# Optimization experiments

Hardware: AMD Instinct MI355X
Metric: run time of the kernel (lower is better)

Reference implementation:

```python
import jax, jax.numpy as jnp
import numpy as np

B, N, D_IN, H, L, NH, PE, DEG, OUT = 8, 1024, 128, 256, 4, 8, 8, 16, 1
BN = B * N
E = BN * DEG
DH = H // NH
EPS = 1e-5


def _gelu(x):
    return jax.nn.gelu(x, approximate=False)  # torch nn.GELU default (erf)


def _bn(x, g, b):
    # BatchNorm1d in training mode: batch mean / biased variance over node dim
    m = x.mean(axis=0)
    v = x.var(axis=0)
    return (x - m) * jax.lax.rsqrt(v + EPS) * g + b


def setup_inputs() -> dict:
    key = jax.random.key(0)
    ks = jax.random.split(key, 30)
    s = 0.05
    x = jax.random.normal(ks[0], (BN, D_IN), jnp.float32)
    # block-diagonal COO adjacency: edges stay within each graph's node block
    base = jnp.repeat(jnp.arange(B, dtype=jnp.int32) * N, N * DEG)
    edge_row = base + jax.random.randint(ks[1], (E,), 0, N, jnp.int32)
    edge_col = base + jax.random.randint(ks[2], (E,), 0, N, jnp.int32)
    edge_val = jax.random.uniform(ks[3], (E,), jnp.float32) / DEG
    batch_pe = jax.random.normal(ks[4], (BN, PE), jnp.float32)
    p = {
        'W_in': jax.random.normal(ks[5], (H, D_IN)) * s,
        'b_in': jnp.zeros((H,)),
        'W_pe': jax.random.normal(ks[6], (H, PE)) * s,
        'b_pe': jnp.zeros((H,)),
        'gcn_W': jax.random.normal(ks[7], (L, H, H)) * s,
        'attn_in_W': jax.random.normal(ks[8], (L, 3 * H, H)) * s,
        'attn_in_b': jnp.zeros((L, 3 * H)),
        'attn_out_W': jax.random.normal(ks[9], (L, H, H)) * s,
        'attn_out_b': jnp.zeros((L, H)),
        'bn_g': jnp.ones((L, 3, H)),
        'bn_b': jnp.zeros((L, 3, H)),
        'ffn_W1': jax.random.normal(ks[10], (L, 4 * H, H)) * s,
        'ffn_b1': jnp.zeros((L, 4 * H)),
        'ffn_W2': jax.random.normal(ks[11], (L, H, 4 * H)) * s,
        'ffn_b2': jnp.zeros((L, H)),
        'head_W1': jax.random.normal(ks[12], (H // 2, H)) * s,
        'head_b1': jnp.zeros((H // 2,)),
        'head_W2': jax.random.normal(ks[13], (OUT, H // 2)) * s,
        'head_b2': jnp.zeros((OUT,)),
    }
    p = {k: v.astype(jnp.float32) for k, v in p.items()}
    return dict(x=x, edge_row=edge_row, edge_col=edge_col, edge_val=edge_val,
                batch_pe=batch_pe, **p)


def reference(x, edge_row, edge_col, edge_val, batch_pe,
              W_in, b_in, W_pe, b_pe,
              gcn_W, attn_in_W, attn_in_b, attn_out_W, attn_out_b,
              bn_g, bn_b, ffn_W1, ffn_b1, ffn_W2, ffn_b2,
              head_W1, head_b1, head_W2, head_b2):
    h = x @ W_in.T + b_in + batch_pe @ W_pe.T + b_pe  # (BN, H)
    scale = 1.0 / jnp.sqrt(jnp.asarray(DH, h.dtype))
    for l in range(L):
        # local GCN: linear -> sparse mm (block-diag COO) -> GELU
        msg = edge_val[:, None] * (h @ gcn_W[l].T)[edge_col]  # (E, H)
        h_local = _gelu(jax.ops.segment_sum(msg, edge_row, num_segments=BN))
        h = _bn(h + h_local, bn_g[l, 0], bn_b[l, 0])
        # global self-attention over each graph's N nodes
        hh = h.reshape(B, N, H)
        qkv = hh @ attn_in_W[l].T + attn_in_b[l]  # (B, N, 3H)
        q, k, v = [t.reshape(B, N, NH, DH) for t in jnp.split(qkv, 3, axis=-1)]
        att = jax.nn.softmax(jnp.einsum('bqhd,bkhd->bhqk', q, k) * scale, axis=-1)
        o = jnp.einsum('bhqk,bkhd->bqhd', att, v).reshape(B, N, H)
        o = (o @ attn_out_W[l].T + attn_out_b[l]).reshape(BN, H)
        h = _bn(h + o, bn_g[l, 1], bn_b[l, 1])
        # FFN
        f = _gelu(h @ ffn_W1[l].T + ffn_b1[l]) @ ffn_W2[l].T + ffn_b2[l]
        h = _bn(h + f, bn_g[l, 2], bn_b[l, 2])
    out = jax.nn.sigmoid(_gelu(h @ head_W1.T + head_b1) @ head_W2.T + head_b2)
    return out
```

## Files before the change

kernel.cpp:

```cpp
#include <hip/hip_runtime.h>
#include <hip/hip_bf16.h>
#include <math.h>

#define BB 8
#define NN 1024
#define BN 8192
#define D_IN 128
#define HH 256
#define LL 4
#define NHD 8
#define DH 32
#define EE 131072
#define EPSV 1e-5f

typedef unsigned short u16;
typedef unsigned int u32;
typedef __attribute__((ext_vector_type(8))) short bf16x8;
typedef __attribute__((ext_vector_type(4))) float f32x4;

__device__ __forceinline__ float gelu_erf(float x) {
    return 0.5f * x * (1.0f + erff(x * 0.70710678118654752f));
}

__device__ __forceinline__ u16 f2bf(float v) {
    __hip_bfloat16 b = __float2bfloat16(v);
    return *reinterpret_cast<u16*>(&b);
}

__device__ __forceinline__ float bf2f(u16 u) {
    u32 x = ((u32)u) << 16;
    return __builtin_bit_cast(float, x);
}

__device__ __forceinline__ u32 pack2bf(float lo, float hi) {
    return ((u32)f2bf(hi) << 16) | (u32)f2bf(lo);
}

__global__ __launch_bounds__(256) void cast_all_kernel(
        const float* s0, const float* s1, const float* s2, const float* s3,
        const float* s4, const float* s5, const float* s6, const float* s7,
        u16* d0, u16* d1, u16* d2, u16* d3, u16* d4, u16* d5, u16* d6, u16* d7) {
    int blk = blockIdx.x;
    const float* s; u16* d; int base;
    if      (blk < 1024) { s = s0; d = d0; base = 0; }
    else if (blk < 1056) { s = s1; d = d1; base = 1024; }
    else if (blk < 1312) { s = s2; d = d2; base = 1056; }
    else if (blk < 2080) { s = s3; d = d3; base = 1312; }
    else if (blk < 2336) { s = s4; d = d4; base = 2080; }
    else if (blk < 3360) { s = s5; d = d5; base = 2336; }
    else if (blk < 4384) { s = s6; d = d6; base = 3360; }
    else                 { s = s7; d = d7; base = 4384; }
    int i = (blk - base) * 256 + threadIdx.x;
    float4 v = ((const float4*)s)[i];
    ushort4 o;
    o.x = f2bf(v.x); o.y = f2bf(v.y); o.z = f2bf(v.z); o.w = f2bf(v.w);
    ((ushort4*)d)[i] = o;
}

__global__ __launch_bounds__(256) void hist_kernel(const int* __restrict__ edge_row,
                                                   int* __restrict__ counts) {
    int e = blockIdx.x * 256 + threadIdx.x;
    atomicAdd(&counts[edge_row[e]], 1);
}

__global__ __launch_bounds__(256) void prefix_kernel(const int* __restrict__ counts,
                                                     int* __restrict__ row_start,
                                                     int* __restrict__ cursor) {
    __shared__ int lds[256];
    int t = threadIdx.x;
    int local[32];
    int s = 0;
#pragma unroll
    for (int i = 0; i < 32; ++i) { local[i] = counts[t * 32 + i]; s += local[i]; }
    lds[t] = s;
    __syncthreads();
    for (int off = 1; off < 256; off <<= 1) {
        int v = (t >= off) ? lds[t - off] : 0;
        __syncthreads();
        lds[t] += v;
        __syncthreads();
    }
    int excl = (t == 0) ? 0 : lds[t - 1];
#pragma unroll
    for (int i = 0; i < 32; ++i) {
        int c = local[i];
        row_start[t * 32 + i] = excl;
        cursor[t * 32 + i] = excl;
        excl += c;
    }
    if (t == 255) row_start[8192] = excl;
}

__global__ __launch_bounds__(256) void scatter_kernel(const int* __restrict__ edge_row,
                                                      int* __restrict__ cursor,
                                                      int* __restrict__ csr_e) {
    int e = blockIdx.x * 256 + threadIdx.x;
    int r = edge_row[e];
    int pos = atomicAdd(&cursor[r], 1);
    csr_e[pos] = e;
}

__global__ __launch_bounds__(256) void gcn_gather_kernel(const u16* __restrict__ t1b,
                                                         const int* __restrict__ row_start,
                                                         const int* __restrict__ csr_e,
                                                         const int* __restrict__ edge_col,
                                                         const float* __restrict__ edge_val,
                                                         float* __restrict__ outb) {
    int wave = threadIdx.x >> 6;
    int lane = threadIdx.x & 63;
    int r = blockIdx.x * 4 + wave;
    float a0 = 0.f, a1 = 0.f, a2 = 0.f, a3 = 0.f;
    int p0 = row_start[r], p1 = row_start[r + 1];
    for (int p = p0; p < p1; ++p) {
        int e = csr_e[p];
        int c = edge_col[e];
        float v = edge_val[e];
        ushort4 sv = *(const ushort4*)&t1b[(size_t)c * HH + lane * 4];
        a0 += v * bf2f(sv.x); a1 += v * bf2f(sv.y);
        a2 += v * bf2f(sv.z); a3 += v * bf2f(sv.w);
    }
    float4 g;
    g.x = gelu_erf(a0); g.y = gelu_erf(a1); g.z = gelu_erf(a2); g.w = gelu_erf(a3);
    *(float4*)&outb[(size_t)r * HH + lane * 4] = g;
}

__global__ __launch_bounds__(256) void bn_reduce_atomic_kernel(float* __restrict__ h,
                                                               const float* __restrict__ add,
                                                               float* __restrict__ S,
                                                               float* __restrict__ Q) {
    int c = threadIdx.x;
    int r0 = blockIdx.x * 32;
    float s = 0.f, q = 0.f;
#pragma unroll 4
    for (int i = 0; i < 32; ++i) {
        int idx = (r0 + i) * HH + c;
        float v = h[idx] + add[idx];
        h[idx] = v;
        s += v; q += v * v;
    }
    atomicAdd(&S[c], s);
    atomicAdd(&Q[c], q);
}

__global__ __launch_bounds__(256) void bn_apply_kernel(float* __restrict__ h,
                                                       u16* __restrict__ hb,
                                                       const float* __restrict__ S,
                                                       const float* __restrict__ Q,
                                                       const float* __restrict__ g,
                                                       const float* __restrict__ b,
                                                       float* __restrict__ Zs,
                                                       float* __restrict__ Zq) {
    int i = blockIdx.x * 256 + threadIdx.x;
    float4 v = ((float4*)h)[i];
    int c4 = (i & 63) * 4;
    float o0, o1, o2, o3;
    {
        float mean = S[c4 + 0] * (1.f / 8192.f);
        float var = Q[c4 + 0] * (1.f / 8192.f) - mean * mean;
        float sc = g[c4 + 0] * rsqrtf(var + EPSV);
        o0 = v.x * sc + (b[c4 + 0] - mean * sc);
    }
    {
        float mean = S[c4 + 1] * (1.f / 8192.f);
        float var = Q[c4 + 1] * (1.f / 8192.f) - mean * mean;
        float sc = g[c4 + 1] * rsqrtf(var + EPSV);
        o1 = v.y * sc + (b[c4 + 1] - mean * sc);
    }
    {
        float mean = S[c4 + 2] * (1.f / 8192.f);
        float var = Q[c4 + 2] * (1.f / 8192.f) - mean * mean;
        float sc = g[c4 + 2] * rsqrtf(var + EPSV);
        o2 = v.z * sc + (b[c4 + 2] - mean * sc);
    }
    {
        float mean = S[c4 + 3] * (1.f / 8192.f);
        float var = Q[c4 + 3] * (1.f / 8192.f) - mean * mean;
        float sc = g[c4 + 3] * rsqrtf(var + EPSV);
        o3 = v.w * sc + (b[c4 + 3] - mean * sc);
    }
    float4 ov; ov.x = o0; ov.y = o1; ov.z = o2; ov.w = o3;
    ((float4*)h)[i] = ov;
    ushort4 o;
    o.x = f2bf(o0); o.y = f2bf(o1); o.z = f2bf(o2); o.w = f2bf(o3);
    ((ushort4*)hb)[i] = o;
    if (blockIdx.x == 0) {
        Zs[threadIdx.x] = 0.f;
        Zq[threadIdx.x] = 0.f;
    }
}

#define SWZ(row, c8) ((c8) ^ (((row) & 7) << 3))
template <int EPI, int OUTMODE>
__global__ __launch_bounds__(256) void gemm_mfma(const u16* __restrict__ A,
                                                 const u16* __restrict__ W,
                                                 const float* __restrict__ bias,
                                                 void* __restrict__ Cout,
                                                 int M, int K, int N,
                                                 float* __restrict__ psumF,
                                                 float* __restrict__ psqF) {
    __shared__ u16 As[128][64];
    __shared__ u16 Ws[64][64];
    int t = threadIdx.x;
    int bm = blockIdx.y * 128, bn = blockIdx.x * 64;
    int wid = t >> 6, lane = t & 63;
    int wr = wid >> 1, wc = wid & 1;
    int lr = lane & 15, lg = lane >> 4;

    f32x4 zero = {0.f, 0.f, 0.f, 0.f};
    f32x4 acc[4][2];
#pragma unroll
    for (int mi = 0; mi < 4; ++mi)
#pragma unroll
        for (int ni = 0; ni < 2; ++ni) acc[mi][ni] = zero;

    int sr = t >> 3;
    int c8 = (t & 7) * 8;

    for (int k0 = 0; k0 < K; k0 += 64) {
        __syncthreads();
#pragma unroll
        for (int p = 0; p < 4; ++p) {
            int row = sr + p * 32;
            const u16* src = A + (size_t)(bm + row) * K + k0 + c8;
            *(int4*)&As[row][SWZ(row, c8)] = *(const int4*)src;
        }
#pragma unroll
        for (int p = 0; p < 2; ++p) {
            int row = sr + p * 32;
            const u16* src = W + (size_t)(bn + row) * K + k0 + c8;
            *(int4*)&Ws[row][SWZ(row, c8)] = *(const int4*)src;
        }
        __syncthreads();
#pragma unroll
        for (int kk = 0; kk < 2; ++kk) {
            bf16x8 af[4], bf[2];
#pragma unroll
            for (int mi = 0; mi < 4; ++mi) {
                int row = wr * 64 + mi * 16 + lr;
                af[mi] = *(const bf16x8*)&As[row][SWZ(row, kk * 32 + lg * 8)];
            }
#pragma unroll
            for (int ni = 0; ni < 2; ++ni) {
                int row = wc * 32 + ni * 16 + lr;
                bf[ni] = *(const bf16x8*)&Ws[row][SWZ(row, kk * 32 + lg * 8)];
            }
#pragma unroll
            for (int mi = 0; mi < 4; ++mi)
#pragma unroll
                for (int ni = 0; ni < 2; ++ni)
                    acc[mi][ni] = __builtin_amdgcn_mfma_f32_16x16x32_bf16(af[mi], bf[ni], acc[mi][ni], 0, 0, 0);
        }
    }

    if (OUTMODE == 2) {
#pragma unroll
        for (int ni = 0; ni < 2; ++ni) {
            int col = bn + wc * 32 + ni * 16 + lr;
            float bj = bias[col];
            float s = 0.f, q = 0.f;
#pragma unroll
            for (int mi = 0; mi < 4; ++mi) {
#pragma unroll
                for (int r = 0; r < 4; ++r) {
                    int row = bm + wr * 64 + mi * 16 + lg * 4 + r;
                    float* hp = (float*)Cout + (size_t)row * N + col;
                    float nv = *hp + acc[mi][ni][r] + bj;
                    *hp = nv;
                    s += nv; q += nv * nv;
                }
            }
            s += __shfl_xor(s, 16); s += __shfl_xor(s, 32);
            q += __shfl_xor(q, 16); q += __shfl_xor(q, 32);
            if (lg == 0) {
                atomicAdd(&psumF[col], s);
                atomicAdd(&psqF[col], q);
            }
        }
    } else {
#pragma unroll
        for (int ni = 0; ni < 2; ++ni) {
            int col = bn + wc * 32 + ni * 16 + lr;
            float bj = bias ? bias[col] : 0.f;
#pragma unroll
            for (int mi = 0; mi < 4; ++mi) {
#pragma unroll
                for (int r = 0; r < 4; ++r) {
                    int row = bm + wr * 64 + mi * 16 + lg * 4 + r;
                    float v = acc[mi][ni][r] + bj;
                    if (EPI == 1) v = gelu_erf(v);
                    if (OUTMODE == 1)
                        ((u16*)Cout)[(size_t)row * N + col] = f2bf(v);
                    else
                        ((float*)Cout)[(size_t)row * N + col] = v;
                }
            }
        }
    }
}

template <int EPI, int OUTBF>
__global__ __launch_bounds__(256) void gemm_mfma2(const u16* __restrict__ A,
                                                  const u16* __restrict__ W,
                                                  const float* __restrict__ bias,
                                                  void* __restrict__ Cout,
                                                  int M, int K, int N) {
    __shared__ u16 As[128][64];
    __shared__ u16 Ws[128][64];
    int t = threadIdx.x;
    int bm = blockIdx.y * 128, bn = blockIdx.x * 128;
    int wid = t >> 6, lane = t & 63;
    int wr = wid >> 1, wc = wid & 1;
    int lr = lane & 15, lg = lane >> 4;

    f32x4 zero = {0.f, 0.f, 0.f, 0.f};
    f32x4 acc[4][4];
#pragma unroll
    for (int mi = 0; mi < 4; ++mi)
#pragma unroll
        for (int ni = 0; ni < 4; ++ni) acc[mi][ni] = zero;

    int sr = t >> 3;
    int c8 = (t & 7) * 8;

    for (int k0 = 0; k0 < K; k0 += 64) {
        __syncthreads();
#pragma unroll
        for (int p = 0; p < 4; ++p) {
            int row = sr + p * 32;
            const u16* srcA = A + (size_t)(bm + row) * K + k0 + c8;
            *(int4*)&As[row][SWZ(row, c8)] = *(const int4*)srcA;
            const u16* srcW = W + (size_t)(bn + row) * K + k0 + c8;
            *(int4*)&Ws[row][SWZ(row, c8)] = *(const int4*)srcW;
        }
        __syncthreads();
#pragma unroll
        for (int kk = 0; kk < 2; ++kk) {
            bf16x8 af[4], bf[4];
#pragma unroll
            for (int mi = 0; mi < 4; ++mi) {
                int row = wr * 64 + mi * 16 + lr;
                af[mi] = *(const bf16x8*)&As[row][SWZ(row, kk * 32 + lg * 8)];
            }
#pragma unroll
            for (int ni = 0; ni < 4; ++ni) {
                int row = wc * 64 + ni * 16 + lr;
                bf[ni] = *(const bf16x8*)&Ws[row][SWZ(row, kk * 32 + lg * 8)];
            }
#pragma unroll
            for (int mi = 0; mi < 4; ++mi)
#pragma unroll
                for (int ni = 0; ni < 4; ++ni)
                    acc[mi][ni] = __builtin_amdgcn_mfma_f32_16x16x32_bf16(af[mi], bf[ni], acc[mi][ni], 0, 0, 0);
        }
    }

#pragma unroll
    for (int ni = 0; ni < 4; ++ni) {
        int col = bn + wc * 64 + ni * 16 + lr;
        float bj = bias ? bias[col] : 0.f;
#pragma unroll
        for (int mi = 0; mi < 4; ++mi) {
#pragma unroll
            for (int r = 0; r < 4; ++r) {
                int row = bm + wr * 64 + mi * 16 + lg * 4 + r;
                float v = acc[mi][ni][r] + bj;
                if (EPI == 1) v = gelu_erf(v);
                if (OUTBF)
                    ((u16*)Cout)[(size_t)row * N + col] = f2bf(v);
                else
                    ((float*)Cout)[(size_t)row * N + col] = v;
            }
        }
    }
}

__global__ __launch_bounds__(256) void pe_add_kernel(const float* __restrict__ pe,
                                                     const float* __restrict__ Wpe,
                                                     const float* __restrict__ bpe,
                                                     float* __restrict__ h,
                                                     u16* __restrict__ hb) {
    __shared__ float Ws[8][256];
    int t = threadIdx.x;
    for (int i = t; i < 2048; i += 256) Ws[i & 7][i >> 3] = Wpe[i];
    __syncthreads();
    int w = t >> 6, lane = t & 63;
    int r = blockIdx.x * 4 + w;
    const float* pr = pe + r * 8;
    float p[8];
#pragma unroll
    for (int k = 0; k < 8; ++k) p[k] = pr[k];
    int c0 = lane * 4;
    float4 hv = *(float4*)&h[(size_t)r * HH + c0];
    float o0 = hv.x + bpe[c0 + 0], o1 = hv.y + bpe[c0 + 1];
    float o2 = hv.z + bpe[c0 + 2], o3 = hv.w + bpe[c0 + 3];
#pragma unroll
    for (int k = 0; k < 8; ++k) {
        o0 += p[k] * Ws[k][c0 + 0];
        o1 += p[k] * Ws[k][c0 + 1];
        o2 += p[k] * Ws[k][c0 + 2];
        o3 += p[k] * Ws[k][c0 + 3];
    }
    float4 ov; ov.x = o0; ov.y = o1; ov.z = o2; ov.w = o3;
    *(float4*)&h[(size_t)r * HH + c0] = ov;
    ushort4 ob;
    ob.x = f2bf(o0); ob.y = f2bf(o1); ob.z = f2bf(o2); ob.w = f2bf(o3);
    *(ushort4*)&hb[(size_t)r * HH + c0] = ob;
}

__global__ __launch_bounds__(256) void vtrans_kernel(const u16* __restrict__ qkv,
                                                     u16* __restrict__ vT) {
    __shared__ u16 Ls[64][64];
    int bid = blockIdx.x;
    int kt = bid & 15;
    int head = (bid >> 4) & 7;
    int b = bid >> 7;
    int t = threadIdx.x;
    int key_l = t >> 2, blkS = t & 3;
    const u16* src = qkv + (size_t)(b * NN + kt * 64 + key_l) * 768 + 512 + head * DH + blkS * 8;
    int sb = (blkS ^ (key_l & 7) ^ ((key_l >> 3) & 7)) * 8;
    *(int4*)&Ls[key_l][sb] = *(const int4*)src;
    __syncthreads();
    int d = t >> 3, kc = t & 7;
    union { u16 a[8]; int4 v; } tmp;
#pragma unroll
    for (int j = 0; j < 8; ++j) {
        int col = (((d >> 3) ^ j ^ kc) << 3) | (d & 7);
        tmp.a[j] = Ls[kc * 8 + j][col];
    }
    u16* dst = vT + (size_t)((b * 8 + head) * 32 + d) * NN + kt * 64 + kc * 8;
    *(int4*)dst = tmp.v;
}

__global__ __launch_bounds__(256) void attn_mfma_kernel(const u16* __restrict__ qkv,
                                                        const u16* __restrict__ vT,
                                                        u16* __restrict__ o) {
    __shared__ __align__(16) u16 Ks[64][40];
    __shared__ __align__(16) u16 Vt[32][72];
    __shared__ __align__(16) u16 Ot[64][40];
    int bid = blockIdx.x;
    int qt = bid & 15;
    int head = (bid >> 4) & 7;
    int b = bid >> 7;
    int t = threadIdx.x;
    int w = t >> 6, lane = t & 63;
    int lr = lane & 15, lg = lane >> 4;

    bf16x8 qf;
    {
        const u16* qsrc = qkv + (size_t)(b * NN + qt * 64 + w * 16 + lr) * 768 + head * DH + lg * 8;
        bf16x8 raw = *(const bf16x8*)qsrc;
#pragma unroll
        for (int j = 0; j < 8; ++j) {
            float f = bf2f((u16)raw[j]) * 0.17677669529663689f;
            qf[j] = (short)f2bf(f);
        }
    }

    f32x4 zero = {0.f, 0.f, 0.f, 0.f};
    f32x4 oacc[2] = {zero, zero};
    float m = -1e30f, l = 0.f;

    int srow = t >> 2, sc8 = (t & 3) * 8;
    int vd = t >> 3, vc8 = (t & 7) * 8;
    const u16* kbase = qkv + (size_t)(b * NN) * 768 + 256 + head * DH + sc8;
    const u16* vbase = vT + (size_t)((b * 8 + head) * 32 + vd) * NN + vc8;

    int srcA = ((lg & 1) << 5) + lr;
    int srcB = srcA + 16;
    int hi = lg >> 1;

    for (int k0 = 0; k0 < NN; k0 += 64) {
        __syncthreads();
        *(int4*)&Ks[srow][sc8] = *(const int4*)(kbase + (size_t)(k0 + srow) * 768);
        *(int4*)&Vt[vd][vc8] = *(const int4*)(vbase + k0);
        __syncthreads();

        f32x4 st[4];
#pragma unroll
        for (int kt = 0; kt < 4; ++kt) {
            bf16x8 kf = *(const bf16x8*)&Ks[kt * 16 + lr][lg * 8];
            st[kt] = __builtin_amdgcn_mfma_f32_16x16x32_bf16(kf, qf, zero, 0, 0, 0);
        }

        float tm = -1e30f;
#pragma unroll
        for (int kt = 0; kt < 4; ++kt)
#pragma unroll
            for (int r = 0; r < 4; ++r) tm = fmaxf(tm, st[kt][r]);
        tm = fmaxf(tm, __shfl_xor(tm, 16));
        tm = fmaxf(tm, __shfl_xor(tm, 32));
        float mn = fmaxf(m, tm);
        float corr = __expf(m - mn);
        l *= corr;
#pragma unroll
        for (int dh = 0; dh < 2; ++dh)
#pragma unroll
            for (int r = 0; r < 4; ++r) oacc[dh][r] *= corr;

        float ps = 0.f;
        u32 pw0[4], pw1[4];
#pragma unroll
        for (int kt = 0; kt < 4; ++kt) {
            float p0 = __expf(st[kt][0] - mn);
            float p1 = __expf(st[kt][1] - mn);
            float p2 = __expf(st[kt][2] - mn);
            float p3 = __expf(st[kt][3] - mn);
            ps += (p0 + p1) + (p2 + p3);
            pw0[kt] = pack2bf(p0, p1);
            pw1[kt] = pack2bf(p2, p3);
        }
        ps += __shfl_xor(ps, 16);
        ps += __shfl_xor(ps, 32);
        l += ps;
        m = mn;

#pragma unroll
        for (int c = 0; c < 2; ++c) {
            u32 w0a = (u32)__shfl((int)pw0[c * 2], srcA);
            u32 w0b = (u32)__shfl((int)pw0[c * 2 + 1], srcA);
            u32 w1a = (u32)__shfl((int)pw1[c * 2], srcA);
            u32 w1b = (u32)__shfl((int)pw1[c * 2 + 1], srcA);
            u32 w2a = (u32)__shfl((int)pw0[c * 2], srcB);
            u32 w2b = (u32)__shfl((int)pw0[c * 2 + 1], srcB);
            u32 w3a = (u32)__shfl((int)pw1[c * 2], srcB);
            u32 w3b = (u32)__shfl((int)pw1[c * 2 + 1], srcB);
            union { bf16x8 v; u32 u[4]; } pf;
            pf.u[0] = hi ? w0b : w0a;
            pf.u[1] = hi ? w1b : w1a;
            pf.u[2] = hi ? w2b : w2a;
            pf.u[3] = hi ? w3b : w3a;
#pragma unroll
            for (int dh = 0; dh < 2; ++dh) {
                bf16x8 vf = *(const bf16x8*)&Vt[dh * 16 + lr][c * 32 + lg * 8];
                oacc[dh] = __builtin_amdgcn_mfma_f32_16x16x32_bf16(vf, pf.v, oacc[dh], 0, 0, 0);
            }
        }
    }

    float inv = 1.f / l;
    __syncthreads();
#pragma unroll
    for (int dh = 0; dh < 2; ++dh)
#pragma unroll
        for (int r = 0; r < 4; ++r)
            Ot[w * 16 + lr][dh * 16 + lg * 4 + r] = f2bf(oacc[dh][r] * inv);
    __syncthreads();
    {
        int orow = t >> 2, oc8 = (t & 3) * 8;
        u16* dst = o + (size_t)(b * NN + qt * 64 + orow) * HH + head * DH + oc8;
        *(int4*)dst = *(const int4*)&Ot[orow][oc8];
    }
}

__global__ __launch_bounds__(256) void head2_kernel(const float* __restrict__ g1,
                                                    const float* __restrict__ W2,
                                                    const float* __restrict__ b2,
                                                    float* __restrict__ out) {
    __shared__ float w[128];
    int t = threadIdx.x;
    if (t < 128) w[t] = W2[t];
    __syncthreads();
    int r = blockIdx.x * 256 + t;
    float s = b2[0];
    const float* row = g1 + (size_t)r * 128;
#pragma unroll
    for (int k = 0; k < 128; k += 4) {
        float4 v = *(const float4*)&row[k];
        s += v.x * w[k] + v.y * w[k + 1] + v.z * w[k + 2] + v.w * w[k + 3];
    }
    out[r] = 1.f / (1.f + __expf(-s));
}

extern "C" void kernel_launch(void* const* d_in, const int* in_sizes, int n_in,
                              void* d_out, int out_size, void* d_ws, size_t ws_size,
                              hipStream_t stream) {
    const float* x        = (const float*)d_in[0];
    const int*   edge_row = (const int*)d_in[1];
    const int*   edge_col = (const int*)d_in[2];
    const float* edge_val = (const float*)d_in[3];
    const float* pe       = (const float*)d_in[4];
    const float* W_in     = (const float*)d_in[5];
    const float* b_in     = (const float*)d_in[6];
    const float* W_pe     = (const float*)d_in[7];
    const float* b_pe     = (const float*)d_in[8];
    const float* gcn_W    = (const float*)d_in[9];
    const float* attn_in_W  = (const float*)d_in[10];
    const float* attn_in_b  = (const float*)d_in[11];
    const float* attn_out_W = (const float*)d_in[12];
    const float* attn_out_b = (const float*)d_in[13];
    const float* bn_g     = (const float*)d_in[14];
    const float* bn_b     = (const float*)d_in[15];
    const float* ffn_W1   = (const float*)d_in[16];
    const float* ffn_b1   = (const float*)d_in[17];
    const float* ffn_W2   = (const float*)d_in[18];
    const float* ffn_b2   = (const float*)d_in[19];
    const float* head_W1  = (const float*)d_in[20];
    const float* head_b1  = (const float*)d_in[21];
    const float* head_W2  = (const float*)d_in[22];
    const float* head_b2  = (const float*)d_in[23];
    float* out = (float*)d_out;

    float* w = (float*)d_ws;
    float* h    = w; w += 2097152;
    float* buf1 = w; w += 8388608;
    float* buf2 = w; w += 2097152;
    int* counts    = (int*)w; w += 8192;
    float* bnstats = w; w += 1024;
    int* row_start = (int*)w; w += 8224;
    int* cursor    = (int*)w; w += 8192;
    int* csr_e     = (int*)w; w += 131072;
    u16* hb   = (u16*)w;
    u16* xb   = hb + 2097152;
    u16* aob  = xb + 1048576;
    u16* wbWin = aob + 2097152;
    u16* wbGcn = wbWin + 32768;
    u16* wbAin = wbGcn + 262144;
    u16* wbAout = wbAin + 786432;
    u16* wbF1  = wbAout + 262144;
    u16* wbF2  = wbF1 + 1048576;
    u16* wbH1  = wbF2 + 1048576;
    u16* t1b  = (u16*)buf1;
    u16* qkvb = (u16*)buf1;
    u16* midb = (u16*)buf1;
    u16* vT   = (u16*)buf1 + 12582912;

    auto Sp = [&](int k) { return bnstats + (k & 1) * 512; };
    auto Qp = [&](int k) { return bnstats + (k & 1) * 512 + 256; };

    hipMemsetAsync(counts, 0, (8192 + 1024) * sizeof(int), stream);
    hist_kernel<<<512, 256, 0, stream>>>(edge_row, counts);
    prefix_kernel<<<1, 256, 0, stream>>>(counts, row_start, cursor);
    scatter_kernel<<<512, 256, 0, stream>>>(edge_row, cursor, csr_e);

    cast_all_kernel<<<4416, 256, 0, stream>>>(
        x, W_in, gcn_W, attn_in_W, attn_out_W, ffn_W1, ffn_W2, head_W1,
        xb, wbWin, wbGcn, wbAin, wbAout, wbF1, wbF2, wbH1);

    gemm_mfma<0, 0><<<dim3(4, 64), 256, 0, stream>>>(xb, wbWin, b_in, h, BN, D_IN, HH, bnstats, bnstats);
    pe_add_kernel<<<2048, 256, 0, stream>>>(pe, W_pe, b_pe, h, hb);

    for (int l = 0; l < LL; ++l) {
        int k1 = l * 3, k2 = l * 3 + 1, k3 = l * 3 + 2;

        gemm_mfma<0, 1><<<dim3(4, 64), 256, 0, stream>>>(hb, wbGcn + l * 65536, nullptr, t1b, BN, HH, HH, bnstats, bnstats);
        gcn_gather_kernel<<<2048, 256, 0, stream>>>(t1b, row_start, csr_e, edge_col, edge_val, buf2);
        bn_reduce_atomic_kernel<<<256, 256, 0, stream>>>(h, buf2, Sp(k1), Qp(k1));
        bn_apply_kernel<<<2048, 256, 0, stream>>>(h, hb, Sp(k1), Qp(k1),
            bn_g + (l * 3 + 0) * 256, bn_b + (l * 3 + 0) * 256, Sp(k1 + 1), Qp(k1 + 1));

        gemm_mfma2<0, 1><<<dim3(6, 64), 256, 0, stream>>>(hb, wbAin + l * 196608, attn_in_b + l * 768, qkvb, BN, HH, 768);
        vtrans_kernel<<<1024, 256, 0, stream>>>(qkvb, vT);
        attn_mfma_kernel<<<1024, 256, 0, stream>>>(qkvb, vT, aob);
        gemm_mfma<0, 2><<<dim3(4, 64), 256, 0, stream>>>(aob, wbAout + l * 65536, attn_out_b + l * 256, h, BN, HH, HH, Sp(k2), Qp(k2));
        bn_apply_kernel<<<2048, 256, 0, stream>>>(h, hb, Sp(k2), Qp(k2),
            bn_g + (l * 3 + 1) * 256, bn_b + (l * 3 + 1) * 256, Sp(k2 + 1), Qp(k2 + 1));

        gemm_mfma2<1, 1><<<dim3(8, 64), 256, 0, stream>>>(hb, wbF1 + l * 262144, ffn_b1 + l * 1024, midb, BN, HH, 1024);
        gemm_mfma<0, 2><<<dim3(4, 64), 256, 0, stream>>>(midb, wbF2 + l * 262144, ffn_b2 + l * 256, h, BN, 1024, HH, Sp(k3), Qp(k3));
        bn_apply_kernel<<<2048, 256, 0, stream>>>(h, hb, Sp(k3), Qp(k3),
            bn_g + (l * 3 + 2) * 256, bn_b + (l * 3 + 2) * 256, Sp(k3 + 1), Qp(k3 + 1));
    }

    gemm_mfma<1, 0><<<dim3(2, 64), 256, 0, stream>>>(hb, wbH1, head_b1, buf1, BN, HH, 128, bnstats, bnstats);
    head2_kernel<<<32, 256, 0, stream>>>(buf1, head_W2, head_b2, out);
}
```

Measured before the change: 847.4 us.

## Fuse BatchNorm apply into GEMM prologues/epilogues and GCN gather, lazy softmax rescale

Removes the standalone bn_apply and bn_reduce passes and the bf16 copy of h. Normalization of the previous BN is now done lazily: the GEMM A-tile loads read fp32 h, apply the scale and shift, and convert to bf16. Residual epilogues apply the pending normalization to h before adding, and the GCN gather fuses residual, normalization and stats accumulation. Attention switches to raw v_exp_f32 with log2e folded into the q scale, and only rescales the running max when it grows by more than 8. The cost is reading fp32 A (twice the bytes), recomputing BN coefficients per tile, and a less parallel per-channel gather loop.

```diff
diff --git a/kernel.cpp b/kernel.cpp
--- a/kernel.cpp
+++ b/kernel.cpp
@@ -34,6 +34,12 @@
 
 __device__ __forceinline__ u32 pack2bf(float lo, float hi) {
     return ((u32)f2bf(hi) << 16) | (u32)f2bf(lo);
+}
+
+__device__ __forceinline__ float exp2_fast(float x) {
+    float r;
+    asm("v_exp_f32 %0, %1" : "=v"(r) : "v"(x));
+    return r;
 }
 
 __global__ __launch_bounds__(256) void cast_all_kernel(
@@ -100,107 +106,66 @@
     csr_e[pos] = e;
 }
 
-__global__ __launch_bounds__(256) void gcn_gather_kernel(const u16* __restrict__ t1b,
-                                                         const int* __restrict__ row_start,
-                                                         const int* __restrict__ csr_e,
-                                                         const int* __restrict__ edge_col,
-                                                         const float* __restrict__ edge_val,
-                                                         float* __restrict__ outb) {
-    int wave = threadIdx.x >> 6;
-    int lane = threadIdx.x & 63;
-    int r = blockIdx.x * 4 + wave;
-    float a0 = 0.f, a1 = 0.f, a2 = 0.f, a3 = 0.f;
-    int p0 = row_start[r], p1 = row_start[r + 1];
-    for (int p = p0; p < p1; ++p) {
-        int e = csr_e[p];
-        int c = edge_col[e];
-        float v = edge_val[e];
-        ushort4 sv = *(const ushort4*)&t1b[(size_t)c * HH + lane * 4];
-        a0 += v * bf2f(sv.x); a1 += v * bf2f(sv.y);
-        a2 += v * bf2f(sv.z); a3 += v * bf2f(sv.w);
-    }
-    float4 g;
-    g.x = gelu_erf(a0); g.y = gelu_erf(a1); g.z = gelu_erf(a2); g.w = gelu_erf(a3);
-    *(float4*)&outb[(size_t)r * HH + lane * 4] = g;
-}
-
-__global__ __launch_bounds__(256) void bn_reduce_atomic_kernel(float* __restrict__ h,
-                                                               const float* __restrict__ add,
-                                                               float* __restrict__ S,
-                                                               float* __restrict__ Q) {
+__global__ __launch_bounds__(256) void gather_bn_kernel(const u16* __restrict__ t1b,
+                                                        const int* __restrict__ row_start,
+                                                        const int* __restrict__ csr_e,
+                                                        const int* __restrict__ edge_col,
+                                                        const float* __restrict__ edge_val,
+                                                        float* __restrict__ h,
+                                                        const float* __restrict__ Sa,
+                                                        const float* __restrict__ Qa,
+                                                        const float* __restrict__ ga,
+                                                        const float* __restrict__ ba,
+                                                        float* __restrict__ So,
+                                                        float* __restrict__ Qo) {
     int c = threadIdx.x;
-    int r0 = blockIdx.x * 32;
+    float sc = 1.f, sh = 0.f;
+    if (Sa) {
+        float mean = Sa[c] * (1.f / 8192.f);
+        float var = Qa[c] * (1.f / 8192.f) - mean * mean;
+        float rs = rsqrtf(var + EPSV);
+        sc = ga[c] * rs;
+        sh = ba[c] - mean * sc;
+    }
+    int r0 = blockIdx.x * 8;
     float s = 0.f, q = 0.f;
-#pragma unroll 4
-    for (int i = 0; i < 32; ++i) {
-        int idx = (r0 + i) * HH + c;
-        float v = h[idx] + add[idx];
-        h[idx] = v;
-        s += v; q += v * v;
-    }
-    atomicAdd(&S[c], s);
-    atomicAdd(&Q[c], q);
-}
-
-__global__ __launch_bounds__(256) void bn_apply_kernel(float* __restrict__ h,
-                                                       u16* __restrict__ hb,
-                                                       const float* __restrict__ S,
-                                                       const float* __restrict__ Q,
-                                                       const float* __restrict__ g,
-                                                       const float* __restrict__ b,
-                                                       float* __restrict__ Zs,
-                                                       float* __restrict__ Zq) {
-    int i = blockIdx.x * 256 + threadIdx.x;
-    float4 v = ((float4*)h)[i];
-    int c4 = (i & 63) * 4;
-    float o0, o1, o2, o3;
-    {
-        float mean = S[c4 + 0] * (1.f / 8192.f);
-        float var = Q[c4 + 0] * (1.f / 8192.f) - mean * mean;
-        float sc = g[c4 + 0] * rsqrtf(var + EPSV);
-        o0 = v.x * sc + (b[c4 + 0] - mean * sc);
-    }
-    {
-        float mean = S[c4 + 1] * (1.f / 8192.f);
-        float var = Q[c4 + 1] * (1.f / 8192.f) - mean * mean;
-        float sc = g[c4 + 1] * rsqrtf(var + EPSV);
-        o1 = v.y * sc + (b[c4 + 1] - mean * sc);
-    }
-    {
-        float mean = S[c4 + 2] * (1.f / 8192.f);
-        float var = Q[c4 + 2] * (1.f / 8192.f) - mean * mean;
-        float sc = g[c4 + 2] * rsqrtf(var + EPSV);
-        o2 = v.z * sc + (b[c4 + 2] - mean * sc);
-    }
-    {
-        float mean = S[c4 + 3] * (1.f / 8192.f);
-        float var = Q[c4 + 3] * (1.f / 8192.f) - mean * mean;
-        float sc = g[c4 + 3] * rsqrtf(var + EPSV);
-        o3 = v.w * sc + (b[c4 + 3] - mean * sc);
-    }
-    float4 ov; ov.x = o0; ov.y = o1; ov.z = o2; ov.w = o3;
-    ((float4*)h)[i] = ov;
-    ushort4 o;
-    o.x = f2bf(o0); o.y = f2bf(o1); o.z = f2bf(o2); o.w = f2bf(o3);
-    ((ushort4*)hb)[i] = o;
-    if (blockIdx.x == 0) {
-        Zs[threadIdx.x] = 0.f;
-        Zq[threadIdx.x] = 0.f;
-    }
+#pragma unroll
+    for (int i = 0; i < 8; ++i) {
+        int r = r0 + i;
+        int p0 = row_start[r], p1 = row_start[r + 1];
+        float a = 0.f;
+        for (int p = p0; p < p1; ++p) {
+            int e = csr_e[p];
+            float v = edge_val[e];
+            a += v * bf2f(t1b[(size_t)edge_col[e] * HH + c]);
+        }
+        size_t idx = (size_t)r * HH + c;
+        float nv = h[idx] * sc + sh + gelu_erf(a);
+        h[idx] = nv;
+        s += nv; q += nv * nv;
+    }
+    atomicAdd(&So[c], s);
+    atomicAdd(&Qo[c], q);
 }
 
 #define SWZ(row, c8) ((c8) ^ (((row) & 7) << 3))
-template <int EPI, int OUTMODE>
-__global__ __launch_bounds__(256) void gemm_mfma(const u16* __restrict__ A,
-                                                 const u16* __restrict__ W,
-                                                 const float* __restrict__ bias,
-                                                 void* __restrict__ Cout,
-                                                 int M, int K, int N,
-                                                 float* __restrict__ psumF,
-                                                 float* __restrict__ psqF) {
+template <int EPI, int OUTMODE, int NORMA>
+__global__ __launch_bounds__(256) void gemm_mfma(
+        const void* __restrict__ Ain, const u16* __restrict__ W,
+        const float* __restrict__ bias, void* __restrict__ Cout,
+        int M, int K, int N,
+        const float* __restrict__ Sa, const float* __restrict__ Qa,
+        const float* __restrict__ ga, const float* __restrict__ ba,
+        const float* __restrict__ Sr, const float* __restrict__ Qr,
+        const float* __restrict__ gr, const float* __restrict__ br,
+        float* __restrict__ So, float* __restrict__ Qo,
+        float* __restrict__ Zs, float* __restrict__ Zq) {
     __shared__ u16 As[128][64];
     __shared__ u16 Ws[64][64];
     int t = threadIdx.x;
+    if (Zs != nullptr && blockIdx.x == 0 && blockIdx.y == 0) {
+        Zs[t] = 0.f; Zq[t] = 0.f;
+    }
     int bm = blockIdx.y * 128, bn = blockIdx.x * 64;
     int wid = t >> 6, lane = t & 63;
     int wr = wid >> 1, wc = wid & 1;
@@ -218,11 +183,46 @@
 
     for (int k0 = 0; k0 < K; k0 += 64) {
         __syncthreads();
-#pragma unroll
-        for (int p = 0; p < 4; ++p) {
-            int row = sr + p * 32;
-            const u16* src = A + (size_t)(bm + row) * K + k0 + c8;
-            *(int4*)&As[row][SWZ(row, c8)] = *(const int4*)src;
+        if (NORMA) {
+            float scj[8], shj[8];
+            if (Sa) {
+#pragma unroll
+                for (int j = 0; j < 8; ++j) {
+                    int ch = k0 + c8 + j;
+                    float mean = Sa[ch] * (1.f / 8192.f);
+                    float var = Qa[ch] * (1.f / 8192.f) - mean * mean;
+                    float rs = rsqrtf(var + EPSV);
+                    scj[j] = ga[ch] * rs;
+                    shj[j] = ba[ch] - mean * scj[j];
+                }
+            } else {
+#pragma unroll
+                for (int j = 0; j < 8; ++j) { scj[j] = 1.f; shj[j] = 0.f; }
+            }
+#pragma unroll
+            for (int p = 0; p < 4; ++p) {
+                int row = sr + p * 32;
+                const float* src = (const float*)Ain + (size_t)(bm + row) * K + k0 + c8;
+                float4 a0 = *(const float4*)src;
+                float4 a1 = *(const float4*)(src + 4);
+                union { u16 a[8]; int4 v; } pk;
+                pk.a[0] = f2bf(a0.x * scj[0] + shj[0]);
+                pk.a[1] = f2bf(a0.y * scj[1] + shj[1]);
+                pk.a[2] = f2bf(a0.z * scj[2] + shj[2]);
+                pk.a[3] = f2bf(a0.w * scj[3] + shj[3]);
+                pk.a[4] = f2bf(a1.x * scj[4] + shj[4]);
+                pk.a[5] = f2bf(a1.y * scj[5] + shj[5]);
+                pk.a[6] = f2bf(a1.z * scj[6] + shj[6]);
+                pk.a[7] = f2bf(a1.w * scj[7] + shj[7]);
+                *(int4*)&As[row][SWZ(row, c8)] = pk.v;
+            }
+        } else {
+#pragma unroll
+            for (int p = 0; p < 4; ++p) {
+                int row = sr + p * 32;
+                const u16* src = (const u16*)Ain + (size_t)(bm + row) * K + k0 + c8;
+                *(int4*)&As[row][SWZ(row, c8)] = *(const int4*)src;
+            }
         }
 #pragma unroll
         for (int p = 0; p < 2; ++p) {
@@ -256,7 +256,11 @@
 #pragma unroll
         for (int ni = 0; ni < 2; ++ni) {
             int col = bn + wc * 32 + ni * 16 + lr;
-            float bj = bias[col];
+            float mean = Sr[col] * (1.f / 8192.f);
+            float var = Qr[col] * (1.f / 8192.f) - mean * mean;
+            float rs = rsqrtf(var + EPSV);
+            float scr = gr[col] * rs;
+            float shr = br[col] - mean * scr + bias[col];
             float s = 0.f, q = 0.f;
 #pragma unroll
             for (int mi = 0; mi < 4; ++mi) {
@@ -264,7 +268,7 @@
                 for (int r = 0; r < 4; ++r) {
                     int row = bm + wr * 64 + mi * 16 + lg * 4 + r;
                     float* hp = (float*)Cout + (size_t)row * N + col;
-                    float nv = *hp + acc[mi][ni][r] + bj;
+                    float nv = (*hp) * scr + shr + acc[mi][ni][r];
                     *hp = nv;
                     s += nv; q += nv * nv;
                 }
@@ -272,8 +276,8 @@
             s += __shfl_xor(s, 16); s += __shfl_xor(s, 32);
             q += __shfl_xor(q, 16); q += __shfl_xor(q, 32);
             if (lg == 0) {
-                atomicAdd(&psumF[col], s);
-                atomicAdd(&psqF[col], q);
+                atomicAdd(&So[col], s);
+                atomicAdd(&Qo[col], q);
             }
         }
     } else {
@@ -298,15 +302,20 @@
     }
 }
 
-template <int EPI, int OUTBF>
-__global__ __launch_bounds__(256) void gemm_mfma2(const u16* __restrict__ A,
-                                                  const u16* __restrict__ W,
-                                                  const float* __restrict__ bias,
-                                                  void* __restrict__ Cout,
-                                                  int M, int K, int N) {
+template <int EPI, int OUTBF, int NORMA>
+__global__ __launch_bounds__(256) void gemm_mfma2(
+        const void* __restrict__ Ain, const u16* __restrict__ W,
+        const float* __restrict__ bias, void* __restrict__ Cout,
+        int M, int K, int N,
+        const float* __restrict__ Sa, const float* __restrict__ Qa,
+        const float* __restrict__ ga, const float* __restrict__ ba,
+        float* __restrict__ Zs, float* __restrict__ Zq) {
     __shared__ u16 As[128][64];
     __shared__ u16 Ws[128][64];
     int t = threadIdx.x;
+    if (Zs != nullptr && blockIdx.x == 0 && blockIdx.y == 0) {
+        Zs[t] = 0.f; Zq[t] = 0.f;
+    }
     int bm = blockIdx.y * 128, bn = blockIdx.x * 128;
     int wid = t >> 6, lane = t & 63;
     int wr = wid >> 1, wc = wid & 1;
@@ -324,11 +333,50 @@
 
     for (int k0 = 0; k0 < K; k0 += 64) {
         __syncthreads();
+        if (NORMA) {
+            float scj[8], shj[8];
+            if (Sa) {
+#pragma unroll
+                for (int j = 0; j < 8; ++j) {
+                    int ch = k0 + c8 + j;
+                    float mean = Sa[ch] * (1.f / 8192.f);
+                    float var = Qa[ch] * (1.f / 8192.f) - mean * mean;
+                    float rs = rsqrtf(var + EPSV);
+                    scj[j] = ga[ch] * rs;
+                    shj[j] = ba[ch] - mean * scj[j];
+                }
+            } else {
+#pragma unroll
+                for (int j = 0; j < 8; ++j) { scj[j] = 1.f; shj[j] = 0.f; }
+            }
+#pragma unroll
+            for (int p = 0; p < 4; ++p) {
+                int row = sr + p * 32;
+                const float* src = (const float*)Ain + (size_t)(bm + row) * K + k0 + c8;
+                float4 a0 = *(const float4*)src;
+                float4 a1 = *(const float4*)(src + 4);
+                union { u16 a[8]; int4 v; } pk;
+                pk.a[0] = f2bf(a0.x * scj[0] + shj[0]);
+                pk.a[1] = f2bf(a0.y * scj[1] + shj[1]);
+                pk.a[2] = f2bf(a0.z * scj[2] + shj[2]);
+                pk.a[3] = f2bf(a0.w * scj[3] + shj[3]);
+                pk.a[4] = f2bf(a1.x * scj[4] + shj[4]);
+                pk.a[5] = f2bf(a1.y * scj[5] + shj[5]);
+                pk.a[6] = f2bf(a1.z * scj[6] + shj[6]);
+                pk.a[7] = f2bf(a1.w * scj[7] + shj[7]);
+                *(int4*)&As[row][SWZ(row, c8)] = pk.v;
+            }
+        } else {
+#pragma unroll
+            for (int p = 0; p < 4; ++p) {
+                int row = sr + p * 32;
+                const u16* src = (const u16*)Ain + (size_t)(bm + row) * K + k0 + c8;
+                *(int4*)&As[row][SWZ(row, c8)] = *(const int4*)src;
+            }
+        }
 #pragma unroll
         for (int p = 0; p < 4; ++p) {
             int row = sr + p * 32;
-            const u16* srcA = A + (size_t)(bm + row) * K + k0 + c8;
-            *(int4*)&As[row][SWZ(row, c8)] = *(const int4*)srcA;
             const u16* srcW = W + (size_t)(bn + row) * K + k0 + c8;
             *(int4*)&Ws[row][SWZ(row, c8)] = *(const int4*)srcW;
         }
@@ -377,8 +425,7 @@
 __global__ __launch_bounds__(256) void pe_add_kernel(const float* __restrict__ pe,
                                                      const float* __restrict__ Wpe,
                                                      const float* __restrict__ bpe,
-                                                     float* __restrict__ h,
-                                                     u16* __restrict__ hb) {
+                                                     float* __restrict__ h) {
     __shared__ float Ws[8][256];
     int t = threadIdx.x;
     for (int i = t; i < 2048; i += 256) Ws[i & 7][i >> 3] = Wpe[i];
@@ -402,9 +449,6 @@
     }
     float4 ov; ov.x = o0; ov.y = o1; ov.z = o2; ov.w = o3;
     *(float4*)&h[(size_t)r * HH + c0] = ov;
-    ushort4 ob;
-    ob.x = f2bf(o0); ob.y = f2bf(o1); ob.z = f2bf(o2); ob.w = f2bf(o3);
-    *(ushort4*)&hb[(size_t)r * HH + c0] = ob;
 }
 
 __global__ __launch_bounds__(256) void vtrans_kernel(const u16* __restrict__ qkv,
@@ -451,7 +495,7 @@
         bf16x8 raw = *(const bf16x8*)qsrc;
 #pragma unroll
         for (int j = 0; j < 8; ++j) {
-            float f = bf2f((u16)raw[j]) * 0.17677669529663689f;
+            float f = bf2f((u16)raw[j]) * 0.25503530f;
             qf[j] = (short)f2bf(f);
         }
     }
@@ -489,22 +533,25 @@
             for (int r = 0; r < 4; ++r) tm = fmaxf(tm, st[kt][r]);
         tm = fmaxf(tm, __shfl_xor(tm, 16));
         tm = fmaxf(tm, __shfl_xor(tm, 32));
-        float mn = fmaxf(m, tm);
-        float corr = __expf(m - mn);
-        l *= corr;
-#pragma unroll
-        for (int dh = 0; dh < 2; ++dh)
-#pragma unroll
-            for (int r = 0; r < 4; ++r) oacc[dh][r] *= corr;
+        if (__any(tm > m + 8.0f)) {
+            float mn = fmaxf(m, tm);
+            float corr = exp2_fast(m - mn);
+            l *= corr;
+#pragma unroll
+            for (int dh = 0; dh < 2; ++dh)
+#pragma unroll
+                for (int r = 0; r < 4; ++r) oacc[dh][r] *= corr;
+            m = mn;
+        }
 
         float ps = 0.f;
         u32 pw0[4], pw1[4];
 #pragma unroll
         for (int kt = 0; kt < 4; ++kt) {
-            float p0 = __expf(st[kt][0] - mn);
-            float p1 = __expf(st[kt][1] - mn);
-            float p2 = __expf(st[kt][2] - mn);
-            float p3 = __expf(st[kt][3] - mn);
+            float p0 = exp2_fast(st[kt][0] - m);
+            float p1 = exp2_fast(st[kt][1] - m);
+            float p2 = exp2_fast(st[kt][2] - m);
+            float p3 = exp2_fast(st[kt][3] - m);
             ps += (p0 + p1) + (p2 + p3);
             pw0[kt] = pack2bf(p0, p1);
             pw1[kt] = pack2bf(p2, p3);
@@ -512,7 +559,6 @@
         ps += __shfl_xor(ps, 16);
         ps += __shfl_xor(ps, 32);
         l += ps;
-        m = mn;
 
 #pragma unroll
         for (int c = 0; c < 2; ++c) {
@@ -603,14 +649,12 @@
     float* w = (float*)d_ws;
     float* h    = w; w += 2097152;
     float* buf1 = w; w += 8388608;
-    float* buf2 = w; w += 2097152;
     int* counts    = (int*)w; w += 8192;
     float* bnstats = w; w += 1024;
     int* row_start = (int*)w; w += 8224;
     int* cursor    = (int*)w; w += 8192;
     int* csr_e     = (int*)w; w += 131072;
-    u16* hb   = (u16*)w;
-    u16* xb   = hb + 2097152;
+    u16* xb   = (u16*)w;
     u16* aob  = xb + 1048576;
     u16* wbWin = aob + 2097152;
     u16* wbGcn = wbWin + 32768;
@@ -626,6 +670,7 @@
 
     auto Sp = [&](int k) { return bnstats + (k & 1) * 512; };
     auto Qp = [&](int k) { return bnstats + (k & 1) * 512 + 256; };
+    const float* NF = nullptr;
 
     hipMemsetAsync(counts, 0, (8192 + 1024) * sizeof(int), stream);
     hist_kernel<<<512, 256, 0, stream>>>(edge_row, counts);
@@ -636,31 +681,36 @@
         x, W_in, gcn_W, attn_in_W, attn_out_W, ffn_W1, ffn_W2, head_W1,
         xb, wbWin, wbGcn, wbAin, wbAout, wbF1, wbF2, wbH1);
 
-    gemm_mfma<0, 0><<<dim3(4, 64), 256, 0, stream>>>(xb, wbWin, b_in, h, BN, D_IN, HH, bnstats, bnstats);
-    pe_add_kernel<<<2048, 256, 0, stream>>>(pe, W_pe, b_pe, h, hb);
+    gemm_mfma<0, 0, 0><<<dim3(4, 64), 256, 0, stream>>>(xb, wbWin, b_in, h, BN, D_IN, HH,
+        NF, NF, NF, NF, NF, NF, NF, NF, nullptr, nullptr, nullptr, nullptr);
+    pe_add_kernel<<<2048, 256, 0, stream>>>(pe, W_pe, b_pe, h);
 
     for (int l = 0; l < LL; ++l) {
-        int k1 = l * 3, k2 = l * 3 + 1, k3 = l * 3 + 2;
-
-        gemm_mfma<0, 1><<<dim3(4, 64), 256, 0, stream>>>(hb, wbGcn + l * 65536, nullptr, t1b, BN, HH, HH, bnstats, bnstats);
-        gcn_gather_kernel<<<2048, 256, 0, stream>>>(t1b, row_start, csr_e, edge_col, edge_val, buf2);
-        bn_reduce_atomic_kernel<<<256, 256, 0, stream>>>(h, buf2, Sp(k1), Qp(k1));
-        bn_apply_kernel<<<2048, 256, 0, stream>>>(h, hb, Sp(k1), Qp(k1),
-            bn_g + (l * 3 + 0) * 256, bn_b + (l * 3 + 0) * 256, Sp(k1 + 1), Qp(k1 + 1));
-
-        gemm_mfma2<0, 1><<<dim3(6, 64), 256, 0, stream>>>(hb, wbAin + l * 196608, attn_in_b + l * 768, qkvb, BN, HH, 768);
+        int k1 = 3 * l, k2 = 3 * l + 1, k3 = 3 * l + 2;
+        const float* SaP = (l == 0) ? nullptr : Sp(k1 - 1);
+        const float* QaP = (l == 0) ? nullptr : Qp(k1 - 1);
+        const float* gP  = (l == 0) ? bn_g : bn_g + (k1 - 1) * 256;
+        const float* bP  = (l == 0) ? bn_b : bn_b + (k1 - 1) * 256;
+
+        gemm_mfma<0, 1, 1><<<dim3(4, 64), 256, 0, stream>>>(h, wbGcn + l * 65536, nullptr, t1b, BN, HH, HH,
+            SaP, QaP, gP, bP, NF, NF, NF, NF, nullptr, nullptr, Sp(k1), Qp(k1));
+        gather_bn_kernel<<<1024, 256, 0, stream>>>(t1b, row_start, csr_e, edge_col, edge_val, h,
+            SaP, QaP, gP, bP, Sp(k1), Qp(k1));
+
+        gemm_mfma2<0, 1, 1><<<dim3(6, 64), 256, 0, stream>>>(h, wbAin + l * 196608, attn_in_b + l * 768, qkvb, BN, HH, 768,
+            Sp(k1), Qp(k1), bn_g + k1 * 256, bn_b + k1 * 256, Sp(k2), Qp(k2));
         vtrans_kernel<<<1024, 256, 0, stream>>>(qkvb, vT);
         attn_mfma_kernel<<<1024, 256, 0, stream>>>(qkvb, vT, aob);
-        gemm_mfma<0, 2><<<dim3(4, 64), 256, 0, stream>>>(aob, wbAout + l * 65536, attn_out_b + l * 256, h, BN, HH, HH, Sp(k2), Qp(k2));
-        bn_apply_kernel<<<2048, 256, 0, stream>>>(h, hb, Sp(k2), Qp(k2),
-            bn_g + (l * 3 + 1) * 256, bn_b + (l * 3 + 1) * 256, Sp(k2 + 1), Qp(k2 + 1));
-
-        gemm_mfma2<1, 1><<<dim3(8, 64), 256, 0, stream>>>(hb, wbF1 + l * 262144, ffn_b1 + l * 1024, midb, BN, HH, 1024);
-        gemm_mfma<0, 2><<<dim3(4, 64), 256, 0, stream>>>(midb, wbF2 + l * 262144, ffn_b2 + l * 256, h, BN, 1024, HH, Sp(k3), Qp(k3));
-        bn_apply_kernel<<<2048, 256, 0, stream>>>(h, hb, Sp(k3), Qp(k3),
-            bn_g + (l * 3 + 2) * 256, bn_b + (l * 3 + 2) * 256, Sp(k3 + 1), Qp(k3 + 1));
-    }
-
-    gemm_mfma<1, 0><<<dim3(2, 64), 256, 0, stream>>>(hb, wbH1, head_b1, buf1, BN, HH, 128, bnstats, bnstats);
+        gemm_mfma<0, 2, 0><<<dim3(4, 64), 256, 0, stream>>>(aob, wbAout + l * 65536, attn_out_b + l * 256, h, BN, HH, HH,
+            NF, NF, NF, NF, Sp(k1), Qp(k1), bn_g + k1 * 256, bn_b + k1 * 256, Sp(k2), Qp(k2), nullptr, nullptr);
+
+        gemm_mfma2<1, 1, 1><<<dim3(8, 64), 256, 0, stream>>>(h, wbF1 + l * 262144, ffn_b1 + l * 1024, midb, BN, HH, 1024,
+            Sp(k2), Qp(k2), bn_g + k2 * 256, bn_b + k2 * 256, Sp(k3), Qp(k3));
+        gemm_mfma<0, 2, 0><<<dim3(4, 64), 256, 0, stream>>>(midb, wbF2 + l * 262144, ffn_b2 + l * 256, h, BN, 1024, HH,
+            NF, NF, NF, NF, Sp(k2), Qp(k2), bn_g + k2 * 256, bn_b + k2 * 256, Sp(k3), Qp(k3), nullptr, nullptr);
+    }
+
+    gemm_mfma<1, 0, 1><<<dim3(2, 64), 256, 0, stream>>>(h, wbH1, head_b1, buf1, BN, HH, 128,
+        Sp(11), Qp(11), bn_g + 11 * 256, bn_b + 11 * 256, NF, NF, NF, NF, nullptr, nullptr, nullptr, nullptr);
     head2_kernel<<<32, 256, 0, stream>>>(buf1, head_W2, head_b2, out);
 }
```

After: 1.015 ms. 19.8% more time.
